# Kernel optimization log

Measured on AMD Instinct MI355X. Metric: run time of the kernel, lower is better.

## Reference

```python
import jax, jax.numpy as jnp
import numpy as np


def setup_inputs() -> dict:
    key = jax.random.key(0)
    k0, k1, k2, k3 = jax.random.split(key, 4)
    B, S, D, F, E = 8, 2048, 1024, 2048, 8
    x = jax.random.normal(k0, (B, S, D), dtype=jnp.float32)
    Wg = jax.random.normal(k1, (D, E), dtype=jnp.float32) * 0.02
    W1 = jax.random.normal(k2, (E, D, F), dtype=jnp.float32) * 0.02
    W2 = jax.random.normal(k3, (E, F, D), dtype=jnp.float32) * 0.02
    return {"x": x, "Wg": Wg, "W1": W1, "W2": W2}


def reference(x, Wg, W1, W2):
    # Expert-choice MoE: experts pick top-C tokens, conflicts resolved by
    # max router prob (ties -> lowest expert index, matching the serial loop).
    B, S, D = x.shape
    E = Wg.shape[1]
    T = B * S
    cap = max(1, T // E)  # capacity_factor = 1.0

    xt = x.reshape(T, D)
    logits = xt @ Wg                      # [T, E]
    probs = jax.nn.softmax(logits, axis=-1)
    pT = probs.T                          # [E, T] token affinities per expert

    _, top_idx = jax.lax.top_k(pT, cap)   # [E, cap] tokens chosen by each expert
    sel = jnp.zeros((E, T), dtype=bool).at[jnp.arange(E)[:, None], top_idx].set(True)

    # Serial conflict loop is equivalent to: per token, pick the selecting
    masked = jnp.where(sel, pT, -jnp.inf)
    assigned = sel.any(axis=0)            # [T]
    tok2exp = jnp.where(assigned,
                        jnp.argmax(masked, axis=0),
                        jnp.argmax(pT, axis=0))          # [T] int
    weights = jnp.take_along_axis(probs, tok2exp[:, None], axis=1)[:, 0]  # [T]

    # Dispatch / expert FFN / weighted combine. Loop over the small fixed
    # expert set; masked tokens contribute exactly zero, matching index_add_.
    out = jnp.zeros_like(xt)
    for e in range(E):
        gate = jnp.where(tok2exp == e, weights, 0.0)     # [T]
        h = jax.nn.gelu(xt @ W1[e], approximate=False) @ W2[e]  # [T, D]
        out = out + gate[:, None] * h

    return out.reshape(B, S, D)
```

## Files before the change

kernel.cpp:

```cpp
#include <hip/hip_runtime.h>
#include <hip/hip_bf16.h>
#include <math.h>

#define T_TOK 16384
#define DIM   1024
#define FF    2048
#define NE    8
#define CAPK  2048
#define WL1SZ 4096
#define WL2SZ 2048
#define NB_W2T 4096

typedef unsigned short u16;
typedef unsigned long long u64;
typedef __attribute__((ext_vector_type(8))) short bf16x8;
typedef __attribute__((ext_vector_type(4))) float f32x4;

__device__ __forceinline__ u16 f2bf(float f) {
  __hip_bfloat16 h = __float2bfloat16(f);
  union { __hip_bfloat16 h; u16 u; } c; c.h = h; return c.u;
}

__device__ __forceinline__ float gelu_f(float v) {
  float z = fabsf(v) * 0.70710678118654752f;
  float t = __builtin_amdgcn_rcpf(1.0f + 0.3275911f * z);
  float poly = t * (0.254829592f +
               t * (-0.284496736f +
               t * (1.421413741f +
               t * (-1.453152027f +
               t * 1.061405429f))));
  float ez = __expf(-z * z);
  float erfz = 1.0f - poly * ez;
  erfz = copysignf(erfz, v);
  return 0.5f * v * (1.0f + erfz);
}

__device__ __forceinline__ void async_copy16(const void* g, void* l) {
  __builtin_amdgcn_global_load_lds(
      (const __attribute__((address_space(1))) unsigned int*)g,
      (__attribute__((address_space(3))) unsigned int*)l, 16, 0, 0);
}

__device__ __forceinline__ bf16x8 ds_read16(const char* p) {
  bf16x8 r;
  asm volatile("ds_read_b128 %0, %1"
               : "=&v"(r)
               : "v"((const __attribute__((address_space(3))) char*)p));
  return r;
}

#define LGKM0()                                                                   \
  do {                                                                            \
    asm volatile("s_waitcnt lgkmcnt(0)" ::: "memory");                            \
    __builtin_amdgcn_sched_barrier(0);                                            \
  } while (0)
#define VMW0() asm volatile("s_waitcnt vmcnt(0)" ::: "memory")
#define BAR() asm volatile("s_barrier" ::: "memory")

__device__ __forceinline__ void transpose_tile(const float* __restrict__ src,
                                               u16* __restrict__ dst, int R, int C,
                                               int bxy, int tid, float (*tile)[65]) {
  int nbx = C >> 6;
  int bx = bxy % nbx, by = bxy / nbx;
  int r0 = by * 64, c0 = bx * 64;
  int lr = tid >> 4, lc4 = (tid & 15) * 4;
#pragma unroll
  for (int p = 0; p < 4; ++p) {
    float4 v = *(const float4*)(src + (size_t)(r0 + p * 16 + lr) * C + c0 + lc4);
    tile[p * 16 + lr][lc4 + 0] = v.x;
    tile[p * 16 + lr][lc4 + 1] = v.y;
    tile[p * 16 + lr][lc4 + 2] = v.z;
    tile[p * 16 + lr][lc4 + 3] = v.w;
  }
  __syncthreads();
  int oc = tid >> 3, orr = (tid & 7) * 8;
#pragma unroll
  for (int p = 0; p < 2; ++p) {
    int c = p * 32 + oc;
    u16 h[8];
#pragma unroll
    for (int j = 0; j < 8; ++j) h[j] = f2bf(tile[orr + j][c]);
    *(uint4*)(dst + (size_t)(c0 + c) * R + r0 + orr) = *(uint4*)h;
  }
}

__global__ __launch_bounds__(256) void prep_k(const float* __restrict__ x,
                                              const float* __restrict__ Wg,
                                              const float* __restrict__ W1,
                                              float* __restrict__ probs,
                                              float* __restrict__ probsT,
                                              u16* __restrict__ xb,
                                              u16* __restrict__ w1t,
                                              u64* __restrict__ key,
                                              int* cnt, int* cnt2, int* gates) {
  __shared__ float tile[64][65];
  int bid = blockIdx.x, tid = threadIdx.x;
  if (bid < 4096) {
    if (tid < 4) key[bid * 4 + tid] = 0ull;
    if (bid == 0 && tid < NE) { cnt[tid] = 0; cnt2[tid] = 0; }
    if (bid == 0 && tid >= 8 && tid < 10) gates[tid - 8] = 0;
    int wid = tid >> 6, lane = tid & 63;
    int t = bid * 4 + wid;
    const float* xr = x + (size_t)t * DIM;
    u16* xbr = xb + (size_t)t * DIM;
    double acc[NE] = {0, 0, 0, 0, 0, 0, 0, 0};
#pragma unroll
    for (int it = 0; it < DIM / 64; ++it) {
      int d = it * 64 + lane;
      float xv = xr[d];
      xbr[d] = f2bf(xv);
      const float4* wrow = (const float4*)(Wg + (size_t)d * NE);
      float4 w0 = wrow[0], w1 = wrow[1];
      acc[0] += (double)xv * (double)w0.x;
      acc[1] += (double)xv * (double)w0.y;
      acc[2] += (double)xv * (double)w0.z;
      acc[3] += (double)xv * (double)w0.w;
      acc[4] += (double)xv * (double)w1.x;
      acc[5] += (double)xv * (double)w1.y;
      acc[6] += (double)xv * (double)w1.z;
      acc[7] += (double)xv * (double)w1.w;
    }
#pragma unroll
    for (int e = 0; e < NE; ++e)
      for (int o = 32; o > 0; o >>= 1) acc[e] += __shfl_down(acc[e], o, 64);
    if (lane == 0) {
      float l[NE], mx = -3.0e38f;
#pragma unroll
      for (int e = 0; e < NE; ++e) { l[e] = (float)acc[e]; mx = fmaxf(mx, l[e]); }
      float s = 0.f;
#pragma unroll
      for (int e = 0; e < NE; ++e) { l[e] = expf(l[e] - mx); s += l[e]; }
      float inv = 1.0f / s;
#pragma unroll
      for (int e = 0; e < NE; ++e) {
        float p = l[e] * inv;
        probs[(size_t)t * NE + e] = p;
        probsT[(size_t)e * T_TOK + t] = p;
      }
    }
  } else {
    int tz = bid - 4096;
    int z = tz >> 9, bxy = tz & 511;
    transpose_tile(W1 + (size_t)z * DIM * FF, w1t + (size_t)z * DIM * FF,
                   DIM, FF, bxy, tid, tile);
  }
}

__global__ __launch_bounds__(256) void moe_route_k(const float* __restrict__ probsT,
                                                   const float* __restrict__ probs,
                                                   u64* __restrict__ key,
                                                   int* __restrict__ tok2exp,
                                                   float* __restrict__ wgt,
                                                   int* cnt, int* cnt2,
                                                   int* __restrict__ list,
                                                   int* basep, int* wl1, int* wl2,
                                                   int* gates) {
  __shared__ float pcol[T_TOK];
  __shared__ unsigned whist[8][2048];
  __shared__ unsigned hist[2048];
  __shared__ unsigned bcast[2];
  __shared__ unsigned wsum[4];
  __shared__ int wps[4];
  int bid = blockIdx.x, tid = threadIdx.x, wid = tid >> 6, lane = tid & 63;
  if (bid < 8) {
    int e = bid;
    const float4* src4 = (const float4*)(probsT + (size_t)e * T_TOK);
    for (int i = tid; i < T_TOK / 4; i += 256) ((float4*)pcol)[i] = src4[i];
    for (int i = tid; i < 8 * 2048; i += 256) ((unsigned*)whist)[i] = 0;
    unsigned prefix = 0, remaining = CAPK;
#pragma unroll 1
    for (int lvl = 0; lvl < 3; ++lvl) {
      int nb = (lvl == 2) ? 1024 : 2048;
      if (lvl == 0) {
        __syncthreads();
        for (int i = tid; i < T_TOK; i += 256)
          atomicAdd(&whist[wid][__float_as_uint(pcol[i]) >> 21], 1u);
        __syncthreads();
        for (int j = tid; j < 2048; j += 256) {
          unsigned s2 = 0;
#pragma unroll
          for (int w = 0; w < 8; ++w) s2 += whist[w][j];
          hist[j] = s2;
        }
        __syncthreads();
      } else {
        for (int i = tid; i < 2048; i += 256) hist[i] = 0;
        __syncthreads();
        for (int i = tid; i < T_TOK; i += 256) {
          unsigned k = __float_as_uint(pcol[i]);
          bool m = (lvl == 1) ? ((k >> 21) == prefix) : ((k >> 10) == prefix);
          if (m) atomicAdd(&hist[(lvl == 1) ? ((k >> 10) & 2047u) : (k & 1023u)], 1u);
        }
        __syncthreads();
      }
      int nper = nb / 256;
      unsigned cv = 0;
      for (int j = 0; j < nper; ++j) cv += hist[tid * nper + j];
      unsigned s = cv;
#pragma unroll
      for (int o = 1; o < 64; o <<= 1) {
        unsigned tv = __shfl_down(s, o, 64);
        if (lane + o < 64) s += tv;
      }
      if (lane == 0) wsum[wid] = s;
      __syncthreads();
      unsigned above = 0;
      for (int w = wid + 1; w < 4; ++w) above += wsum[w];
      unsigned Sincl = s + above, Sexcl = Sincl - cv;
      if (Sincl >= remaining && Sexcl < remaining) {
        unsigned rem2 = remaining - Sexcl, cum2 = 0;
        for (int j = nper - 1; j >= 0; --j) {
          unsigned h = hist[tid * nper + j];
          if (cum2 + h >= rem2) { bcast[0] = (unsigned)(tid * nper + j); bcast[1] = rem2 - cum2; break; }
          cum2 += h;
        }
      }
      __syncthreads();
      unsigned b = bcast[0];
      remaining = bcast[1];
      prefix = (lvl == 0) ? b : (lvl == 1) ? ((prefix << 11) | b) : ((prefix << 10) | b);
      __syncthreads();
    }
    unsigned vk = prefix;
    int need = (int)remaining;
    const int CH = T_TOK / 256;
    int i0 = tid * CH;
    int myt = 0;
    for (int i = i0; i < i0 + CH; ++i)
      myt += (__float_as_uint(pcol[i]) == vk);
    int p = myt;
#pragma unroll
    for (int o = 1; o < 64; o <<= 1) {
      int tv = __shfl_up(p, o, 64);
      if (lane >= o) p += tv;
    }
    if (lane == 63) wps[wid] = p;
    __syncthreads();
    int wo = 0;
    for (int w = 0; w < wid; ++w) wo += wps[w];
    int run = wo + p - myt;
    u64 ebits = (u64)(7 - e);
    for (int i = i0; i < i0 + CH; ++i) {
      unsigned k = __float_as_uint(pcol[i]);
      bool sv = false;
      if (k > vk) sv = true;
      else if (k == vk) { if (run < need) sv = true; run++; }
      if (sv) atomicMax(&key[i], ((u64)k << 3) | ebits);
    }
    __threadfence();
    __syncthreads();
    if (tid == 0) atomicAdd(&gates[0], 1);
  } else {
    if (tid == 0) {
      while (atomicAdd(&gates[0], 0) < 8) __builtin_amdgcn_s_sleep(8);
    }
    __syncthreads();
    __threadfence();
    int gid = (bid - 8) * 256 + tid;
    u64 k = key[gid];
    int best;
    float bp;
    if (k) {
      best = 7 - (int)(k & 7);
      bp = __uint_as_float((unsigned)(k >> 3));
    } else {
      best = 0; bp = -3.0e38f;
#pragma unroll
      for (int e = 0; e < NE; ++e) {
        float p = probs[(size_t)gid * NE + e];
        if (p > bp) { bp = p; best = e; }
      }
    }
    tok2exp[gid] = best;
    wgt[gid] = bp;
#pragma unroll
    for (int e = 0; e < NE; ++e) {
      u64 m = __ballot(best == e);
      if (best == e && lane == __ffsll(m) - 1) atomicAdd(&cnt[e], (int)__popcll(m));
    }
    __threadfence();
    __syncthreads();
    if (tid == 0) atomicAdd(&gates[1], 1);
    if (tid == 0) {
      while (atomicAdd(&gates[1], 0) < 64) __builtin_amdgcn_s_sleep(8);
    }
    __syncthreads();
    __threadfence();
    int c[NE];
#pragma unroll
    for (int e = 0; e < NE; ++e) c[e] = cnt[e];
    if (gid < NE) {
      int r = 0;
      for (int e = 0; e < gid; ++e) r += c[e];
      basep[gid] = r;
    }
    if (gid < WL1SZ) {
      int e = gid & 7, j = gid >> 3;
      int mte = (c[e] + 127) >> 7;
      wl1[gid] = (j < mte * 16) ? (e | ((j >> 4) << 4) | ((j & 15) << 12)) : -1;
    }
    if (gid >= WL1SZ && gid < WL1SZ + WL2SZ) {
      int g2 = gid - WL1SZ;
      int e = g2 & 7, j = g2 >> 3;
      int mte = (c[e] + 127) >> 7;
      wl2[g2] = (j < mte * 8) ? (e | ((j >> 3) << 4) | ((j & 7) << 12)) : -1;
    }
    int te = tok2exp[gid];
    int bp_e = 0;
#pragma unroll
    for (int e = 0; e < NE; ++e) if (e < te) bp_e += c[e];
    int sl = 0;
#pragma unroll
    for (int e = 0; e < NE; ++e) {
      u64 m = __ballot(te == e);
      if (te == e) {
        int leader = __ffsll(m) - 1;
        int rank = __popcll(m & ((1ull << lane) - 1));
        int b = 0;
        if (lane == leader) b = atomicAdd(&cnt2[e], (int)__popcll(m));
        b = __shfl(b, leader, 64);
        sl = bp_e + b + rank;
      }
    }
    list[sl] = gid;
  }
}


#define MF(M, N_, AV, BV) acc[M][N_] = __builtin_amdgcn_mfma_f32_16x16x32_bf16(BV, AV, acc[M][N_], 0, 0, 0)

#define STG(kt)                                                                   \
  do {                                                                            \
    char* dA = sm;                                                                \
    char* dB = sm + 16384;                                                        \
    size_t ko = (size_t)(kt) * 128;                                               \
    async_copy16(aP0 + ko,      dA + tid * 16);                                   \
    async_copy16(aP1 + ko,      dA + 4096 + tid * 16);                            \
    async_copy16(aP0 + ko + 64, dA + 8192 + tid * 16);                            \
    async_copy16(aP1 + ko + 64, dA + 12288 + tid * 16);                           \
    async_copy16(bP0 + ko,      dB + tid * 16);                                   \
    async_copy16(bP1 + ko,      dB + 4096 + tid * 16);                            \
    async_copy16(bP0 + ko + 64, dB + 8192 + tid * 16);                            \
    async_copy16(bP1 + ko + 64, dB + 12288 + tid * 16);                           \
  } while (0)

#define DSRD(kkoff)                                                               \
  do {                                                                            \
    const char* pa = sm + (kkoff) + wr * 4096 + laneOff;                          \
    const char* pb = sm + 16384 + (kkoff) + wc * 4096 + laneOff;                  \
    a0 = ds_read16(pa);        a1 = ds_read16(pa + 1024);                         \
    a2 = ds_read16(pa + 2048); a3 = ds_read16(pa + 3072);                         \
    b0 = ds_read16(pb);        b1 = ds_read16(pb + 1024);                         \
    b2 = ds_read16(pb + 2048); b3 = ds_read16(pb + 3072);                         \
  } while (0)

#define MFMA16()                                                                  \
  do {                                                                            \
    __builtin_amdgcn_s_setprio(1);                                                \
    MF(0, 0, a0, b0); MF(0, 1, a0, b1); MF(0, 2, a0, b2); MF(0, 3, a0, b3);       \
    MF(1, 0, a1, b0); MF(1, 1, a1, b1); MF(1, 2, a1, b2); MF(1, 3, a1, b3);       \
    MF(2, 0, a2, b0); MF(2, 1, a2, b1); MF(2, 2, a2, b2); MF(2, 3, a2, b3);       \
    MF(3, 0, a3, b0); MF(3, 1, a3, b1); MF(3, 2, a3, b2); MF(3, 3, a3, b3);       \
    __builtin_amdgcn_s_setprio(0);                                                \
  } while (0)

template <int EPI>
__global__ __launch_bounds__(256, 4) void ffn_k(const u16* __restrict__ A,
                                                const u16* __restrict__ Bm,
                                                void* __restrict__ Out,
                                                const int* __restrict__ list,
                                                const float* __restrict__ wgt,
                                                const int* __restrict__ basep,
                                                const int* __restrict__ cnt,
                                                const int* __restrict__ wl,
                                                const float* __restrict__ W2f,
                                                u16* __restrict__ w2t) {
  constexpr int K = EPI ? FF : DIM;
  constexpr int N = EPI ? DIM : FF;
  constexpr int KT = K / 64;

  __shared__ u16 smem[16384];
  __shared__ int toks[128];
  __shared__ float wsc[128];
  char* const sm = (char*)smem;
  const int tid = threadIdx.x;

  if (EPI == 0 && blockIdx.x >= WL1SZ) {
    int tz = blockIdx.x - WL1SZ;
    int z = tz >> 9, bxy = tz & 511;
    transpose_tile(W2f + (size_t)z * FF * DIM, w2t + (size_t)z * FF * DIM,
                   FF, DIM, bxy, tid, (float (*)[65])sm);
    return;
  }

  const int wle = wl[blockIdx.x];
  if (wle < 0) return;
  const int e = wle & 15, mt = (wle >> 4) & 255, nt = wle >> 12;
  const int ce = cnt[e];
  const int be = basep[e];

  if (tid < 128) {
    int r = mt * 128 + tid;
    int tk = (r < ce) ? list[be + r] : list[be];
    toks[tid] = tk;
    if (EPI == 1) wsc[tid] = wgt[tk];
  }
  __syncthreads();

  const int wid = tid >> 6, lane = tid & 63;
  const int wr = wid >> 1, wc = wid & 1;
  const int laneOff = ((lane & 15) >> 1) * 128 + (lane & 1) * 64 +
                      (((lane >> 4) << 4) ^ ((((lane & 15) >> 1) & 3) << 4));

  const int r0 = 2 * (tid >> 3) + ((tid & 7) >> 2);
  const int cbl = ((tid & 3) << 4) ^ (((tid >> 3) & 3) << 4);
  const char *aP0, *aP1;
  if (EPI == 0) {
    aP0 = (const char*)(A + (size_t)toks[r0] * K) + cbl;
    aP1 = (const char*)(A + (size_t)toks[r0 + 64] * K) + cbl;
  } else {
    aP0 = (const char*)(A + ((size_t)be + mt * 128 + r0) * K) + cbl;
    aP1 = (const char*)(A + ((size_t)be + mt * 128 + r0 + 64) * K) + cbl;
  }
  const char* bP0 = (const char*)(Bm + ((size_t)e * N + nt * 128 + r0) * K) + cbl;
  const char* bP1 = (const char*)(Bm + ((size_t)e * N + nt * 128 + r0 + 64) * K) + cbl;

  f32x4 acc[4][4];
#pragma unroll
  for (int m = 0; m < 4; ++m)
#pragma unroll
    for (int n = 0; n < 4; ++n) acc[m][n] = (f32x4){0.f, 0.f, 0.f, 0.f};

  bf16x8 a0, a1, a2, a3, b0, b1, b2, b3;

#pragma unroll 1
  for (int kt = 0; kt < KT; ++kt) {
    STG(kt);
    VMW0();
    BAR();
    DSRD(0);
    LGKM0();
    MFMA16();
    DSRD(8192);
    LGKM0();
    MFMA16();
    BAR();
  }

  const int lc = lane & 15, lq = (lane >> 4) * 4;
#pragma unroll
  for (int m = 0; m < 4; ++m) {
    int trow = wr * 64 + m * 16 + lc;
    int grow = mt * 128 + trow;
    if (grow < ce) {
      if (EPI == 0) {
        size_t rowoff = (size_t)(be + grow) * FF + nt * 128 + wc * 64 + lq;
#pragma unroll
        for (int n = 0; n < 4; ++n) {
          ushort4 h4;
          h4.x = f2bf(gelu_f(acc[m][n][0]));
          h4.y = f2bf(gelu_f(acc[m][n][1]));
          h4.z = f2bf(gelu_f(acc[m][n][2]));
          h4.w = f2bf(gelu_f(acc[m][n][3]));
          *(ushort4*)((u16*)Out + rowoff + n * 16) = h4;
        }
      } else {
        float w = wsc[trow];
        size_t rowoff = (size_t)toks[trow] * DIM + nt * 128 + wc * 64 + lq;
#pragma unroll
        for (int n = 0; n < 4; ++n) {
          float4 o = make_float4(w * acc[m][n][0], w * acc[m][n][1],
                                 w * acc[m][n][2], w * acc[m][n][3]);
          *(float4*)((float*)Out + rowoff + n * 16) = o;
        }
      }
    }
  }
}

extern "C" void kernel_launch(void* const* d_in, const int* in_sizes, int n_in,
                              void* d_out, int out_size, void* d_ws, size_t ws_size,
                              hipStream_t stream) {
  (void)in_sizes; (void)n_in; (void)out_size; (void)ws_size;
  const float* x  = (const float*)d_in[0];
  const float* Wg = (const float*)d_in[1];
  const float* W1 = (const float*)d_in[2];
  const float* W2 = (const float*)d_in[3];
  float* out = (float*)d_out;

  char* ws = (char*)d_ws;
  size_t off = 0;
  auto alloc = [&](size_t bytes) -> void* {
    void* p = ws + off;
    off += (bytes + 255) & ~(size_t)255;
    return p;
  };
  u16* xb   = (u16*)alloc((size_t)T_TOK * DIM * 2);
  u16* w1t  = (u16*)alloc((size_t)NE * FF * DIM * 2);
  u16* w2t  = (u16*)alloc((size_t)NE * DIM * FF * 2);
  u16* H    = (u16*)alloc((size_t)(T_TOK + 256) * FF * 2);
  float* probs  = (float*)alloc((size_t)T_TOK * NE * 4);
  float* probsT = (float*)alloc((size_t)NE * T_TOK * 4);
  u64* key      = (u64*)alloc((size_t)T_TOK * 8);
  float* wgt    = (float*)alloc((size_t)T_TOK * 4);
  int* tok2exp  = (int*)alloc((size_t)T_TOK * 4);
  int* list     = (int*)alloc((size_t)T_TOK * 4);
  int* cnt      = (int*)alloc(64);
  int* cnt2     = (int*)alloc(64);
  int* basep    = (int*)alloc(64);
  int* gates    = (int*)alloc(64);
  int* wl1      = (int*)alloc(WL1SZ * 4);
  int* wl2      = (int*)alloc(WL2SZ * 4);

  prep_k<<<4096 + 4096, 256, 0, stream>>>(x, Wg, W1, probs, probsT, xb, w1t,
                                          key, cnt, cnt2, gates);
  moe_route_k<<<72, 256, 0, stream>>>(probsT, probs, key, tok2exp, wgt, cnt, cnt2,
                                      list, basep, wl1, wl2, gates);
  ffn_k<0><<<WL1SZ + NB_W2T, 256, 0, stream>>>(xb, w1t, H, list, wgt, basep, cnt, wl1,
                                               W2, w2t);
  ffn_k<1><<<WL2SZ, 256, 0, stream>>>(H, w2t, out, list, wgt, basep, cnt, wl2,
                                      W2, w2t);
}
```

Before: 350.6 us.

## Fuse routing top-k and assignment into prep kernel with global gates

Merges the separate routing kernel into the prep kernel. The top-k and assignment blocks are appended after the router and W1 transpose blocks and wait on atomic gate counters, and a tiny init kernel zeroes the gates. The top-k radix select changes from 11/11/10-bit levels to four 8-bit levels and reads probsT straight from global memory instead of staging it in a 64KB LDS buffer. This is meant to remove a launch boundary and let top-k overlap the W1 transpose, but it relies on the gated blocks being scheduled after the blocks they wait on, which is a deadlock risk and adds an extra radix pass.

```diff
diff --git a/kernel.cpp b/kernel.cpp
--- a/kernel.cpp
+++ b/kernel.cpp
@@ -10,6 +10,12 @@
 #define WL1SZ 4096
 #define WL2SZ 2048
 #define NB_W2T 4096
+
+#define NB_ROUTER 4096
+#define NB_W1T    4096
+#define NB_TOPK   8
+#define NB_ASSIGN 64
+#define PREP_NB (NB_ROUTER + NB_W1T + NB_TOPK + NB_ASSIGN)
 
 typedef unsigned short u16;
 typedef unsigned long long u64;
@@ -57,6 +63,10 @@
 #define VMW0() asm volatile("s_waitcnt vmcnt(0)" ::: "memory")
 #define BAR() asm volatile("s_barrier" ::: "memory")
 
+__global__ void init0_k(int* gates) {
+  if (threadIdx.x < 8) gates[threadIdx.x] = 0;
+}
+
 __device__ __forceinline__ void transpose_tile(const float* __restrict__ src,
                                                u16* __restrict__ dst, int R, int C,
                                                int bxy, int tid, float (*tile)[65]) {
@@ -92,14 +102,19 @@
                                               u16* __restrict__ xb,
                                               u16* __restrict__ w1t,
                                               u64* __restrict__ key,
-                                              int* cnt, int* cnt2, int* gates) {
-  __shared__ float tile[64][65];
+                                              int* __restrict__ tok2exp,
+                                              float* __restrict__ wgt,
+                                              int* cnt, int* cnt2,
+                                              int* __restrict__ list,
+                                              int* basep, int* wl1, int* wl2,
+                                              int* gates) {
+  __shared__ char shm[17472];
   int bid = blockIdx.x, tid = threadIdx.x;
-  if (bid < 4096) {
+  int wid = tid >> 6, lane = tid & 63;
+
+  if (bid < NB_ROUTER) {
     if (tid < 4) key[bid * 4 + tid] = 0ull;
     if (bid == 0 && tid < NE) { cnt[tid] = 0; cnt2[tid] = 0; }
-    if (bid == 0 && tid >= 8 && tid < 10) gates[tid - 8] = 0;
-    int wid = tid >> 6, lane = tid & 63;
     int t = bid * 4 + wid;
     const float* xr = x + (size_t)t * DIM;
     u16* xbr = xb + (size_t)t * DIM;
@@ -138,64 +153,55 @@
         probsT[(size_t)e * T_TOK + t] = p;
       }
     }
-  } else {
-    int tz = bid - 4096;
+    __threadfence();
+    __syncthreads();
+    if (tid == 0) atomicAdd(&gates[0], 1);
+
+  } else if (bid < NB_ROUTER + NB_W1T) {
+    int tz = bid - NB_ROUTER;
     int z = tz >> 9, bxy = tz & 511;
     transpose_tile(W1 + (size_t)z * DIM * FF, w1t + (size_t)z * DIM * FF,
-                   DIM, FF, bxy, tid, tile);
-  }
-}
-
-__global__ __launch_bounds__(256) void moe_route_k(const float* __restrict__ probsT,
-                                                   const float* __restrict__ probs,
-                                                   u64* __restrict__ key,
-                                                   int* __restrict__ tok2exp,
-                                                   float* __restrict__ wgt,
-                                                   int* cnt, int* cnt2,
-                                                   int* __restrict__ list,
-                                                   int* basep, int* wl1, int* wl2,
-                                                   int* gates) {
-  __shared__ float pcol[T_TOK];
-  __shared__ unsigned whist[8][2048];
-  __shared__ unsigned hist[2048];
-  __shared__ unsigned bcast[2];
-  __shared__ unsigned wsum[4];
-  __shared__ int wps[4];
-  int bid = blockIdx.x, tid = threadIdx.x, wid = tid >> 6, lane = tid & 63;
-  if (bid < 8) {
-    int e = bid;
-    const float4* src4 = (const float4*)(probsT + (size_t)e * T_TOK);
-    for (int i = tid; i < T_TOK / 4; i += 256) ((float4*)pcol)[i] = src4[i];
-    for (int i = tid; i < 8 * 2048; i += 256) ((unsigned*)whist)[i] = 0;
+                   DIM, FF, bxy, tid, (float (*)[65])shm);
+
+  } else if (bid < NB_ROUTER + NB_W1T + NB_TOPK) {
+    unsigned* whist = (unsigned*)shm;
+    unsigned* hist  = (unsigned*)(shm + 16384);
+    unsigned* bcast = (unsigned*)(shm + 17408);
+    unsigned* wsum  = (unsigned*)(shm + 17424);
+    int*      wps   = (int*)(shm + 17440);
+    if (tid == 0) {
+      while (atomicAdd(&gates[0], 0) < NB_ROUTER) __builtin_amdgcn_s_sleep(8);
+    }
+    __syncthreads();
+    __threadfence();
+    int e = bid - (NB_ROUTER + NB_W1T);
+    const float* pT = probsT + (size_t)e * T_TOK;
     unsigned prefix = 0, remaining = CAPK;
 #pragma unroll 1
-    for (int lvl = 0; lvl < 3; ++lvl) {
-      int nb = (lvl == 2) ? 1024 : 2048;
+    for (int lvl = 0; lvl < 4; ++lvl) {
+      int shift = 24 - 8 * lvl;
+      unsigned cv;
       if (lvl == 0) {
+        for (int i = tid; i < 16 * 256; i += 256) whist[i] = 0;
         __syncthreads();
+        int sub = wid * 4 + (lane & 3);
         for (int i = tid; i < T_TOK; i += 256)
-          atomicAdd(&whist[wid][__float_as_uint(pcol[i]) >> 21], 1u);
+          atomicAdd(&whist[sub * 256 + (__float_as_uint(pT[i]) >> 24)], 1u);
         __syncthreads();
-        for (int j = tid; j < 2048; j += 256) {
-          unsigned s2 = 0;
-#pragma unroll
-          for (int w = 0; w < 8; ++w) s2 += whist[w][j];
-          hist[j] = s2;
+        cv = 0;
+#pragma unroll
+        for (int w = 0; w < 16; ++w) cv += whist[w * 256 + tid];
+      } else {
+        hist[tid] = 0;
+        __syncthreads();
+        for (int i = tid; i < T_TOK; i += 256) {
+          unsigned k = __float_as_uint(pT[i]);
+          if ((k >> (shift + 8)) == prefix)
+            atomicAdd(&hist[(k >> shift) & 255u], 1u);
         }
         __syncthreads();
-      } else {
-        for (int i = tid; i < 2048; i += 256) hist[i] = 0;
-        __syncthreads();
-        for (int i = tid; i < T_TOK; i += 256) {
-          unsigned k = __float_as_uint(pcol[i]);
-          bool m = (lvl == 1) ? ((k >> 21) == prefix) : ((k >> 10) == prefix);
-          if (m) atomicAdd(&hist[(lvl == 1) ? ((k >> 10) & 2047u) : (k & 1023u)], 1u);
-        }
-        __syncthreads();
-      }
-      int nper = nb / 256;
-      unsigned cv = 0;
-      for (int j = 0; j < nper; ++j) cv += hist[tid * nper + j];
+        cv = hist[tid];
+      }
       unsigned s = cv;
 #pragma unroll
       for (int o = 1; o < 64; o <<= 1) {
@@ -208,17 +214,12 @@
       for (int w = wid + 1; w < 4; ++w) above += wsum[w];
       unsigned Sincl = s + above, Sexcl = Sincl - cv;
       if (Sincl >= remaining && Sexcl < remaining) {
-        unsigned rem2 = remaining - Sexcl, cum2 = 0;
-        for (int j = nper - 1; j >= 0; --j) {
-          unsigned h = hist[tid * nper + j];
-          if (cum2 + h >= rem2) { bcast[0] = (unsigned)(tid * nper + j); bcast[1] = rem2 - cum2; break; }
-          cum2 += h;
-        }
+        bcast[0] = (unsigned)tid;
+        bcast[1] = remaining - Sexcl;
       }
       __syncthreads();
-      unsigned b = bcast[0];
+      prefix = (prefix << 8) | bcast[0];
       remaining = bcast[1];
-      prefix = (lvl == 0) ? b : (lvl == 1) ? ((prefix << 11) | b) : ((prefix << 10) | b);
       __syncthreads();
     }
     unsigned vk = prefix;
@@ -227,7 +228,7 @@
     int i0 = tid * CH;
     int myt = 0;
     for (int i = i0; i < i0 + CH; ++i)
-      myt += (__float_as_uint(pcol[i]) == vk);
+      myt += (__float_as_uint(pT[i]) == vk);
     int p = myt;
 #pragma unroll
     for (int o = 1; o < 64; o <<= 1) {
@@ -241,7 +242,7 @@
     int run = wo + p - myt;
     u64 ebits = (u64)(7 - e);
     for (int i = i0; i < i0 + CH; ++i) {
-      unsigned k = __float_as_uint(pcol[i]);
+      unsigned k = __float_as_uint(pT[i]);
       bool sv = false;
       if (k > vk) sv = true;
       else if (k == vk) { if (run < need) sv = true; run++; }
@@ -249,14 +250,15 @@
     }
     __threadfence();
     __syncthreads();
-    if (tid == 0) atomicAdd(&gates[0], 1);
+    if (tid == 0) atomicAdd(&gates[1], 1);
+
   } else {
     if (tid == 0) {
-      while (atomicAdd(&gates[0], 0) < 8) __builtin_amdgcn_s_sleep(8);
+      while (atomicAdd(&gates[1], 0) < NB_TOPK) __builtin_amdgcn_s_sleep(8);
     }
     __syncthreads();
     __threadfence();
-    int gid = (bid - 8) * 256 + tid;
+    int gid = (bid - (NB_ROUTER + NB_W1T + NB_TOPK)) * 256 + tid;
     u64 k = key[gid];
     int best;
     float bp;
@@ -280,9 +282,9 @@
     }
     __threadfence();
     __syncthreads();
-    if (tid == 0) atomicAdd(&gates[1], 1);
+    if (tid == 0) atomicAdd(&gates[2], 1);
     if (tid == 0) {
-      while (atomicAdd(&gates[1], 0) < 64) __builtin_amdgcn_s_sleep(8);
+      while (atomicAdd(&gates[2], 0) < NB_ASSIGN) __builtin_amdgcn_s_sleep(8);
     }
     __syncthreads();
     __threadfence();
@@ -512,9 +514,9 @@
   int* wl1      = (int*)alloc(WL1SZ * 4);
   int* wl2      = (int*)alloc(WL2SZ * 4);
 
-  prep_k<<<4096 + 4096, 256, 0, stream>>>(x, Wg, W1, probs, probsT, xb, w1t,
-                                          key, cnt, cnt2, gates);
-  moe_route_k<<<72, 256, 0, stream>>>(probsT, probs, key, tok2exp, wgt, cnt, cnt2,
+  init0_k<<<1, 64, 0, stream>>>(gates);
+  prep_k<<<PREP_NB, 256, 0, stream>>>(x, Wg, W1, probs, probsT, xb, w1t,
+                                      key, tok2exp, wgt, cnt, cnt2,
                                       list, basep, wl1, wl2, gates);
   ffn_k<0><<<WL1SZ + NB_W2T, 256, 0, stream>>>(xb, w1t, H, list, wgt, basep, cnt, wl1,
                                                W2, w2t);
```

Result: slower. 949.0 us (+170.7%).

## Double-buffer LDS with K-step 32 to overlap global loads and MFMA

Applied to the files above, without the earlier changes.

Splits the 32 KB LDS into two 16 KB buffers, each holding one K=32 slice of A and B. The next slice is prefetched asynchronously while the current one feeds the MFMAs, so global-memory latency overlaps compute instead of stalling behind a wait at the start of every iteration. In exchange, each iteration does half the MFMA work, so the number of barriers and loop iterations doubles. The lane offsets and XOR swizzle are reworked to match the new 64-byte row stride.

```diff
diff --git a/kernel.cpp b/kernel.cpp
--- a/kernel.cpp
+++ b/kernel.cpp
@@ -329,25 +329,20 @@
 
 #define MF(M, N_, AV, BV) acc[M][N_] = __builtin_amdgcn_mfma_f32_16x16x32_bf16(BV, AV, acc[M][N_], 0, 0, 0)
 
-#define STG(kt)                                                                   \
+#define STG(b, kt)                                                                \
   do {                                                                            \
-    char* dA = sm;                                                                \
-    char* dB = sm + 16384;                                                        \
-    size_t ko = (size_t)(kt) * 128;                                               \
-    async_copy16(aP0 + ko,      dA + tid * 16);                                   \
-    async_copy16(aP1 + ko,      dA + 4096 + tid * 16);                            \
-    async_copy16(aP0 + ko + 64, dA + 8192 + tid * 16);                            \
-    async_copy16(aP1 + ko + 64, dA + 12288 + tid * 16);                           \
-    async_copy16(bP0 + ko,      dB + tid * 16);                                   \
-    async_copy16(bP1 + ko,      dB + 4096 + tid * 16);                            \
-    async_copy16(bP0 + ko + 64, dB + 8192 + tid * 16);                            \
-    async_copy16(bP1 + ko + 64, dB + 12288 + tid * 16);                           \
+    char* base = sm + (b) * 16384;                                                \
+    size_t ko = (size_t)(kt) * 64;                                                \
+    async_copy16(aP0 + ko, base + tid * 16);                                      \
+    async_copy16(aP1 + ko, base + 4096 + tid * 16);                               \
+    async_copy16(bP0 + ko, base + 8192 + tid * 16);                               \
+    async_copy16(bP1 + ko, base + 12288 + tid * 16);                              \
   } while (0)
 
-#define DSRD(kkoff)                                                               \
+#define DSRD(b)                                                                   \
   do {                                                                            \
-    const char* pa = sm + (kkoff) + wr * 4096 + laneOff;                          \
-    const char* pb = sm + 16384 + (kkoff) + wc * 4096 + laneOff;                  \
+    const char* pa = sm + (b) * 16384 + wr * 4096 + laneOff;                      \
+    const char* pb = sm + (b) * 16384 + 8192 + wc * 4096 + laneOff;               \
     a0 = ds_read16(pa);        a1 = ds_read16(pa + 1024);                         \
     a2 = ds_read16(pa + 2048); a3 = ds_read16(pa + 3072);                         \
     b0 = ds_read16(pb);        b1 = ds_read16(pb + 1024);                         \
@@ -377,7 +372,7 @@
                                                 u16* __restrict__ w2t) {
   constexpr int K = EPI ? FF : DIM;
   constexpr int N = EPI ? DIM : FF;
-  constexpr int KT = K / 64;
+  constexpr int KT = K / 32;
 
   __shared__ u16 smem[16384];
   __shared__ int toks[128];
@@ -409,11 +404,11 @@
 
   const int wid = tid >> 6, lane = tid & 63;
   const int wr = wid >> 1, wc = wid & 1;
-  const int laneOff = ((lane & 15) >> 1) * 128 + (lane & 1) * 64 +
-                      (((lane >> 4) << 4) ^ ((((lane & 15) >> 1) & 3) << 4));
-
-  const int r0 = 2 * (tid >> 3) + ((tid & 7) >> 2);
-  const int cbl = ((tid & 3) << 4) ^ (((tid >> 3) & 3) << 4);
+  const int laneOff = (lane & 15) * 64 +
+                      (((lane >> 4) ^ (((lane & 15) >> 1) & 3)) << 4);
+
+  const int r0 = tid >> 2;
+  const int cbl = (((tid & 3) ^ ((tid >> 3) & 3)) << 4);
   const char *aP0, *aP1;
   if (EPI == 0) {
     aP0 = (const char*)(A + (size_t)toks[r0] * K) + cbl;
@@ -433,17 +428,18 @@
 
   bf16x8 a0, a1, a2, a3, b0, b1, b2, b3;
 
+  STG(0, 0);
+  VMW0();
+  BAR();
+
 #pragma unroll 1
   for (int kt = 0; kt < KT; ++kt) {
-    STG(kt);
-    VMW0();
-    BAR();
-    DSRD(0);
+    const int cb = kt & 1, nb = cb ^ 1;
+    if (kt + 1 < KT) STG(nb, kt + 1);
+    DSRD(cb);
     LGKM0();
     MFMA16();
-    DSRD(8192);
-    LGKM0();
-    MFMA16();
+    VMW0();
     BAR();
   }
 
```

New measurement: 372.9 us. +6.4%, slower.
